# Kernel optimization log

Measured on AMD Instinct MI355X. Metric: run time of the kernel, lower is better.

Reference implementation:

```python
import jax, jax.numpy as jnp
import numpy as np

B, N, DIM, VDIM, H, HD = 4, 1369, 1024, 1536, 16, 64
ROPE_HW, ROPE_DIM, THETA = 37, 32, 10000.0
LN_EPS = 1e-5


def _rope_tables():
    # VisionRotaryEmbeddingFast: freqs_for='lang', dim=32, pt_seq_len=ft_seq_len=37
    inv = 1.0 / THETA ** (jnp.arange(0, ROPE_DIM, 2, dtype=jnp.float32) / ROPE_DIM)  # [16]
    t = jnp.arange(ROPE_HW, dtype=jnp.float32) / ROPE_HW * ROPE_HW                    # [37]
    f = t[:, None] * inv[None, :]                                                     # [37,16]
    f = jnp.repeat(f, 2, axis=-1)                                                     # [37,32]
    # broadcat along last dim over the 2D grid -> [37,37,64]
    f2 = jnp.concatenate([jnp.broadcast_to(f[:, None, :], (ROPE_HW, ROPE_HW, ROPE_DIM)),
                          jnp.broadcast_to(f[None, :, :], (ROPE_HW, ROPE_HW, ROPE_DIM))], axis=-1)
    f2 = f2.reshape(-1, 2 * ROPE_DIM)                                                 # [1369,64]
    return jnp.cos(f2), jnp.sin(f2)


def _rotate_half(x):
    # pairs (x0,x1) -> (-x1,x0), interleaved
    xr = x.reshape(*x.shape[:-1], x.shape[-1] // 2, 2)
    x1, x2 = xr[..., 0], xr[..., 1]
    return jnp.stack((-x2, x1), axis=-1).reshape(x.shape)


def setup_inputs() -> dict:
    key = jax.random.key(0)
    ks = jax.random.split(key, 8)
    return {
        "x": jax.random.normal(ks[0], (B, N, DIM), jnp.float32),
        "value": jax.random.normal(ks[1], (B, N, VDIM), jnp.float32),
        "attn_mask": jax.random.randint(ks[2], (B, N), 0, 2).astype(bool),
        "wq": jax.random.normal(ks[3], (DIM, DIM), jnp.float32) * 0.02,
        "wk": jax.random.normal(ks[4], (DIM, VDIM), jnp.float32) * 0.02,
        "wv": jax.random.normal(ks[5], (DIM, VDIM), jnp.float32) * 0.02,
        "ln_g": jnp.ones((DIM,), jnp.float32),
        "ln_b": jnp.zeros((DIM,), jnp.float32),
        "wp": jax.random.normal(ks[6], (DIM, DIM), jnp.float32) * 0.02,
        "bp": jnp.zeros((DIM,), jnp.float32),
    }


def reference(x, value, attn_mask, wq, wk, wv, ln_g, ln_b, wp, bp):
    cos, sin = _rope_tables()  # [N, 64] each
    # projections (torch F.linear: y = x @ W.T)
    q = jnp.einsum('bni,oi->bno', x, wq).reshape(B, N, H, HD).transpose(0, 2, 1, 3)
    k = jnp.einsum('bni,oi->bno', value, wk).reshape(B, N, H, HD).transpose(0, 2, 1, 3)
    v = jnp.einsum('bni,oi->bno', value, wv).reshape(B, N, H, HD).transpose(0, 2, 1, 3)
    # inline RoPE on q and k
    q = q * cos + _rotate_half(q) * sin
    k = k * cos + _rotate_half(k) * sin
    q = q * (HD ** -0.5)
    attn = jnp.einsum('bhnd,bhmd->bhnm', q, k)
    neg_inf = jnp.finfo(attn.dtype).min
    attn = jnp.where(attn_mask[:, None, None, :], attn, neg_inf)
    attn = jax.nn.softmax(attn, axis=-1)
    out = jnp.einsum('bhnm,bhmd->bhnd', attn, v)
    out = out.transpose(0, 2, 1, 3).reshape(B, N, H * HD)
    # inner_attn_ln (LayerNorm, eps=1e-5)
    mu = jnp.mean(out, axis=-1, keepdims=True)
    var = jnp.var(out, axis=-1, keepdims=True)
    out = (out - mu) * jax.lax.rsqrt(var + LN_EPS) * ln_g + ln_b
    # output projection
    return jnp.einsum('bni,oi->bno', out, wp) + bp
```

## Files before the change

kernel.cpp:

```cpp
#include <hip/hip_runtime.h>
#include <hip/hip_bf16.h>

#define BB 4
#define NN 1369
#define DIMM 1024
#define VDIMM 1536
#define HH 16
#define MM (BB*NN)
#define MPAD 5504
#define MPAD2 5632
#define NPAD 1408
#define KVB 64
#define NT (NPAD/KVB)
#define QSCALE 0.18028334f

typedef __attribute__((ext_vector_type(4))) float f32x4;
typedef __attribute__((ext_vector_type(8))) __bf16 bf16x8;
typedef __attribute__((ext_vector_type(4))) __bf16 bf16x4;

#define GLOAD_LDS(gsrc, ldst) \
  __builtin_amdgcn_global_load_lds((const __attribute__((address_space(1))) unsigned int*)(gsrc), \
                                   (__attribute__((address_space(3))) unsigned int*)(ldst), 16, 0, 0)

__global__ __launch_bounds__(256) void cvt_inputs(const float* __restrict__ x,
                                                  const float* __restrict__ val,
                                                  __bf16* __restrict__ xb,
                                                  __bf16* __restrict__ vb) {
  const int NX = MM * 1024 / 4;
  const int NV = MM * 1536 / 4;
  int i = blockIdx.x * blockDim.x + threadIdx.x;
  int st = gridDim.x * blockDim.x;
  for (; i < NX + NV; i += st) {
    const float* s; __bf16* d; int j;
    if (i < NX) { s = x; d = xb; j = i; }
    else        { s = val; d = vb; j = i - NX; }
    f32x4 v = ((const f32x4*)s)[j];
    bf16x4 o;
    o[0] = (__bf16)v[0]; o[1] = (__bf16)v[1];
    o[2] = (__bf16)v[2]; o[3] = (__bf16)v[3];
    ((bf16x4*)d)[j] = o;
  }
}

__global__ __launch_bounds__(256) void cvt_weights(
    const float* __restrict__ wq, const float* __restrict__ wk,
    const float* __restrict__ wv, const float* __restrict__ wp,
    const float* __restrict__ g,
    __bf16* __restrict__ wqb, __bf16* __restrict__ wkvb, __bf16* __restrict__ wgb) {
  const int NQ = 1024 * 1024 / 4;
  const int NK = 1024 * 1536 / 4;
  int i = blockIdx.x * blockDim.x + threadIdx.x;
  int st = gridDim.x * blockDim.x;
  for (; i < 2 * NQ + 2 * NK; i += st) {
    int j = i;
    if (j < NQ) {
      f32x4 v = ((const f32x4*)wq)[j];
      bf16x4 o;
      o[0] = (__bf16)v[0]; o[1] = (__bf16)v[1]; o[2] = (__bf16)v[2]; o[3] = (__bf16)v[3];
      ((bf16x4*)wqb)[j] = o;
    } else if (j < NQ + NK) {
      j -= NQ;
      f32x4 v = ((const f32x4*)wk)[j];
      bf16x4 o;
      o[0] = (__bf16)v[0]; o[1] = (__bf16)v[1]; o[2] = (__bf16)v[2]; o[3] = (__bf16)v[3];
      ((bf16x4*)wkvb)[j] = o;
    } else if (j < NQ + 2 * NK) {
      j -= NQ + NK;
      f32x4 v = ((const f32x4*)wv)[j];
      bf16x4 o;
      o[0] = (__bf16)v[0]; o[1] = (__bf16)v[1]; o[2] = (__bf16)v[2]; o[3] = (__bf16)v[3];
      ((bf16x4*)(wkvb + (size_t)1024 * 1536))[j] = o;
    } else {
      j -= NQ + 2 * NK;
      f32x4 v = ((const f32x4*)wp)[j];
      f32x4 gv = ((const f32x4*)g)[j & 255];
      bf16x4 o;
      o[0] = (__bf16)(v[0] * gv[0]); o[1] = (__bf16)(v[1] * gv[1]);
      o[2] = (__bf16)(v[2] * gv[2]); o[3] = (__bf16)(v[3] * gv[3]);
      ((bf16x4*)wgb)[j] = o;
    }
  }
}

__global__ __launch_bounds__(256) void c12_kernel(
    const float* __restrict__ wp, const float* __restrict__ g,
    const float* __restrict__ lnb, const float* __restrict__ bpv,
    float* __restrict__ c1, float* __restrict__ c2) {
  const int w = threadIdx.x >> 6, l = threadIdx.x & 63;
  const int o = blockIdx.x * 4 + w;
  const float* row = wp + (size_t)o * 1024;
  float s1 = 0.f, s2 = 0.f;
#pragma unroll
  for (int j = 0; j < 4; ++j) {
    const int idx = l * 4 + j * 256;
    f32x4 wv = *(const f32x4*)&row[idx];
    f32x4 gv = *(const f32x4*)&g[idx];
    f32x4 bv = *(const f32x4*)&lnb[idx];
#pragma unroll
    for (int e = 0; e < 4; ++e) { s1 += wv[e] * gv[e]; s2 += wv[e] * bv[e]; }
  }
#pragma unroll
  for (int m = 1; m < 64; m <<= 1) { s1 += __shfl_xor(s1, m); s2 += __shfl_xor(s2, m); }
  if (l == 0) { c1[o] = s1; c2[o] = s2 + bpv[o]; }
}

__global__ __launch_bounds__(256) void stats_kernel(
    const __bf16* __restrict__ AO, float* __restrict__ mu, float* __restrict__ rstd) {
  const int w = threadIdx.x >> 6, l = threadIdx.x & 63;
  const int row = blockIdx.x * 4 + w;
  const __bf16* x = AO + (size_t)row * DIMM + l * 16;
  float s = 0.f, sq = 0.f;
#pragma unroll
  for (int j = 0; j < 2; ++j) {
    bf16x8 v = *(const bf16x8*)&x[j * 8];
#pragma unroll
    for (int e = 0; e < 8; ++e) { float f = (float)v[e]; s += f; sq += f * f; }
  }
#pragma unroll
  for (int m = 1; m < 64; m <<= 1) { s += __shfl_xor(s, m); sq += __shfl_xor(sq, m); }
  if (l == 0) {
    float mean = s * (1.f / 1024.f);
    mu[row] = mean;
    rstd[row] = rsqrtf(sq * (1.f / 1024.f) - mean * mean + 1e-5f);
  }
}

__global__ __launch_bounds__(256) void prep_aux(float* __restrict__ cosT,
                                                float* __restrict__ sinT,
                                                const void* __restrict__ mask,
                                                float* __restrict__ maskA) {
  const int blk = blockIdx.x;
  if (blk < 343) {
    int idx = blk * 256 + threadIdx.x;
    if (idx >= NN * 64) return;
    int n = idx >> 6, d = idx & 63;
    int r = n / 37, c = n % 37;
    int m = (d < 32) ? (d >> 1) : ((d - 32) >> 1);
    float p = (d < 32) ? (float)r : (float)c;
    float inv = powf(10000.f, -(float)m * (1.f / 16.f));
    float a = p * inv;
    cosT[idx] = cosf(a);
    sinT[idx] = sinf(a);
  } else {
    __shared__ int flags[2];
    int t = threadIdx.x;
    if (t < 2) flags[t] = 0;
    __syncthreads();
    const unsigned int* mw = (const unsigned int*)mask;
    for (int i = t; i < NN; i += blockDim.x) {
      unsigned int w = mw[i];
      if (w == 0x3F800000u) atomicOr(&flags[1], 1);
      else if (w > 1u) atomicOr(&flags[0], 1);
    }
    __syncthreads();
    int md = flags[1] ? 2 : (flags[0] ? 1 : 0);
    const unsigned char* mb = (const unsigned char*)mask;
    const float* mf = (const float*)mask;
    for (int i = t; i < BB * NPAD; i += blockDim.x) {
      int b = i / NPAD, key = i % NPAD;
      float v = -1e30f;
      if (key < NN) {
        int idx = b * NN + key;
        bool on = (md == 0) ? (mw[idx] != 0u) : (md == 1) ? (mb[idx] != 0) : (mf[idx] != 0.f);
        if (on) v = 0.f;
      }
      maskA[i] = v;
    }
  }
}

__global__ __launch_bounds__(512, 2) void gemm_kv256(
    const __bf16* __restrict__ A, const __bf16* __restrict__ W,
    __bf16* __restrict__ Kb, __bf16* __restrict__ Vtb,
    const float* __restrict__ cosT, const float* __restrict__ sinT) {
  __shared__ __bf16 Ar[4][256 * 32];
  __shared__ __bf16 Br[4][256 * 32];
  const int tid = threadIdx.x;
  const int wid = tid >> 6, l = tid & 63;
  const int wr = wid >> 2, wc = wid & 3;
  const int lo = l & 15, hi = l >> 4;
  const int tN = blockIdx.x & 7, tM = blockIdx.x >> 3;
  const int K = VDIMM;
  const int nk = K / 32;

  const int srow = (tid >> 6) * 16 + (tid & 15);
  const int schunk = ((tid >> 4) & 3) * 8;
  const __bf16* Asrc = A + (size_t)(tM * 256 + srow) * K + schunk;
  const __bf16* Wsrc = W + (size_t)(tN * 256 + srow) * K + schunk;

  f32x4 zero = {0.f, 0.f, 0.f, 0.f};
  f32x4 acc[8][4];
#pragma unroll
  for (int i = 0; i < 8; ++i)
#pragma unroll
    for (int j = 0; j < 4; ++j) acc[i][j] = zero;

  auto GSTAGE = [&](int s, int k0) {
    GLOAD_LDS(Asrc + k0,                (char*)&Ar[s][0] + tid * 16);
    GLOAD_LDS(Asrc + (size_t)128 * K + k0, (char*)&Ar[s][0] + tid * 16 + 8192);
    GLOAD_LDS(Wsrc + k0,                (char*)&Br[s][0] + tid * 16);
    GLOAD_LDS(Wsrc + (size_t)128 * K + k0, (char*)&Br[s][0] + tid * 16 + 8192);
  };

  GSTAGE(0, 0);
  GSTAGE(1, 32);
  for (int t = 0; t < nk; ++t) {
    if (t < nk - 1) asm volatile("s_waitcnt vmcnt(4)" ::: "memory");
    else            asm volatile("s_waitcnt vmcnt(0)" ::: "memory");
    __builtin_amdgcn_s_barrier();
    const int s = t & 3;
    bf16x8 af[8], bf[4];
#pragma unroll
    for (int mi = 0; mi < 8; ++mi)
      af[mi] = *(const bf16x8*)&Ar[s][(wr * 8 + mi) * 512 + hi * 128 + lo * 8];
#pragma unroll
    for (int ni = 0; ni < 4; ++ni)
      bf[ni] = *(const bf16x8*)&Br[s][(wc * 4 + ni) * 512 + hi * 128 + lo * 8];
    if (t + 2 < nk) GSTAGE((t + 2) & 3, (t + 2) * 32);
    __builtin_amdgcn_s_setprio(1);
#pragma unroll
    for (int mi = 0; mi < 8; ++mi)
#pragma unroll
      for (int ni = 0; ni < 4; ++ni)
        acc[mi][ni] = __builtin_amdgcn_mfma_f32_16x16x32_bf16(af[mi], bf[ni], acc[mi][ni], 0, 0, 0);
    __builtin_amdgcn_s_setprio(0);
  }

  const int m_base = tM * 256 + wr * 128;
  const int o_base = tN * 256 + wc * 64;
  const bool isK = (tN < 4);
#pragma unroll
  for (int mi = 0; mi < 8; ++mi) {
    const int m4 = m_base + mi * 16 + hi * 4;
    if (!isK) {
      if (m4 < MM) {
        const int b0 = m4 / NN, n0 = m4 % NN;
#pragma unroll
        for (int ni = 0; ni < 4; ++ni) {
          const int o2 = o_base + ni * 16 + lo - 1024;
          const int h = o2 >> 6, d = o2 & 63;
          if (n0 <= NN - 4) {
            bf16x4 pv;
#pragma unroll
            for (int r = 0; r < 4; ++r) pv[r] = (__bf16)acc[mi][ni][r];
            *(bf16x4*)&Vtb[((size_t)(b0 * HH + h) * 64 + d) * NPAD + n0] = pv;
          } else {
#pragma unroll
            for (int r = 0; r < 4; ++r) {
              const int mr = m4 + r;
              const int br = mr / NN, nr = mr % NN;
              Vtb[((size_t)(br * HH + h) * 64 + d) * NPAD + nr] = (__bf16)acc[mi][ni][r];
            }
          }
        }
      }
    } else {
#pragma unroll
      for (int r = 0; r < 4; ++r) {
        const int mrow = m4 + r;
#pragma unroll
        for (int ni = 0; ni < 4; ++ni) {
          const int col = o_base + ni * 16 + lo;
          float v = acc[mi][ni][r];
          float pprt = __shfl_xor(v, 1);
          if (mrow < MM) {
            int b = mrow / NN, n = mrow % NN;
            int h = col >> 6, d = col & 63;
            float cs = cosT[n * 64 + d], sn = sinT[n * 64 + d];
            float out = v * cs + (((d & 1) == 0) ? -pprt : pprt) * sn;
            Kb[((size_t)(b * HH + h) * NPAD + n) * 64 + d] = (__bf16)out;
          }
        }
      }
    }
  }
}

template <int EPI>
__global__ __launch_bounds__(256) void gemm_bt(
    const __bf16* __restrict__ A, const __bf16* __restrict__ W, int K,
    __bf16* __restrict__ obf, float* __restrict__ of32,
    const float* __restrict__ cosT, const float* __restrict__ sinT,
    const float* __restrict__ mu, const float* __restrict__ rstd,
    const float* __restrict__ c1, const float* __restrict__ c2) {
  __shared__ __bf16 As[2][128 * 32];
  __shared__ __bf16 Bs[2][64 * 32];
  const int tid = threadIdx.x;
  const int w = tid >> 6, l = tid & 63;
  const int tN = blockIdx.x, tM = blockIdx.y;
  const int wmo = w * 32;
  const int lo = l & 15, hi = l >> 4;

  const __bf16* Asrc = A + (size_t)(tM * 128 + lo) * K + hi * 8;
  const __bf16* Wsrc = W + (size_t)(tN * 64 + lo) * K + hi * 8;

  f32x4 zero = {0.f, 0.f, 0.f, 0.f};
  f32x4 acc[2][4];
#pragma unroll
  for (int i = 0; i < 2; ++i)
#pragma unroll
    for (int j = 0; j < 4; ++j) acc[i][j] = zero;

  auto GSTAGE = [&](int buf, int k0) {
#pragma unroll
    for (int j = 0; j < 2; ++j) {
      const int c = j * 4 + w;
      GLOAD_LDS(Asrc + (size_t)c * 16 * K + k0, (char*)&As[buf][c * 512]);
    }
    GLOAD_LDS(Wsrc + (size_t)w * 16 * K + k0, (char*)&Bs[buf][w * 512]);
  };

  const int nk = K >> 5;
  GSTAGE(0, 0);
  int cur = 0;
  const int ga = wmo >> 4;
  for (int t = 0; t < nk; ++t) {
    __syncthreads();
    if (t + 1 < nk) GSTAGE(cur ^ 1, (t + 1) * 32);
    bf16x8 af[2], bfr[4];
#pragma unroll
    for (int mi = 0; mi < 2; ++mi)
      af[mi] = *(const bf16x8*)&As[cur][(ga + mi) * 512 + hi * 128 + lo * 8];
#pragma unroll
    for (int ni = 0; ni < 4; ++ni)
      bfr[ni] = *(const bf16x8*)&Bs[cur][ni * 512 + hi * 128 + lo * 8];
    __builtin_amdgcn_s_setprio(1);
#pragma unroll
    for (int mi = 0; mi < 2; ++mi)
#pragma unroll
      for (int ni = 0; ni < 4; ++ni)
        acc[mi][ni] = __builtin_amdgcn_mfma_f32_16x16x32_bf16(af[mi], bfr[ni], acc[mi][ni], 0, 0, 0);
    __builtin_amdgcn_s_setprio(0);
    cur ^= 1;
  }

  const int m_base = tM * 128 + wmo;
  const int o_base = tN * 64;
  float c1v[4], c2v[4];
  if (EPI == 3) {
#pragma unroll
    for (int ni = 0; ni < 4; ++ni) {
      c1v[ni] = c1[o_base + ni * 16 + lo];
      c2v[ni] = c2[o_base + ni * 16 + lo];
    }
  }
#pragma unroll
  for (int mi = 0; mi < 2; ++mi) {
#pragma unroll
    for (int r = 0; r < 4; ++r) {
      const int mrow = m_base + mi * 16 + hi * 4 + r;
#pragma unroll
      for (int ni = 0; ni < 4; ++ni) {
        const int col = o_base + ni * 16 + lo;
        float v = acc[mi][ni][r];
        if (EPI == 0) {
          float pprt = __shfl_xor(v, 1);
          if (mrow < MM) {
            int b = mrow / NN, n = mrow % NN;
            int h = col >> 6, d = col & 63;
            float cs = cosT[n * 64 + d], sn = sinT[n * 64 + d];
            float out = (v * cs + (((d & 1) == 0) ? -pprt : pprt) * sn) * QSCALE;
            obf[((size_t)(b * HH + h) * NPAD + n) * 64 + d] = (__bf16)out;
          }
        } else {
          if (mrow < MM)
            of32[(size_t)mrow * DIMM + col] =
                rstd[mrow] * (v - mu[mrow] * c1v[ni]) + c2v[ni];
        }
      }
    }
  }
}

__device__ inline unsigned int pk2(float a, float b) {
  unsigned int ua = (unsigned int)__builtin_bit_cast(unsigned short, (__bf16)a);
  unsigned int ub = (unsigned int)__builtin_bit_cast(unsigned short, (__bf16)b);
  return ua | (ub << 16);
}

__global__ __launch_bounds__(256) void attn_kernel(
    const __bf16* __restrict__ Qb, const __bf16* __restrict__ Kb,
    const __bf16* __restrict__ Vtb, const float* __restrict__ maskA,
    __bf16* __restrict__ AO) {
  __shared__ __bf16 Ks[2][64 * 64];
  __shared__ __bf16 Vs[2][64 * 64];
  __shared__ unsigned int Plds[4][16 * 32];
  const int tid = threadIdx.x;
  const int w = tid >> 6, l = tid & 63;
  const int lo = l & 15, hi = l >> 4;

  const int i = blockIdx.x;
  const int orig = (i & 7) * 176 + (i >> 3);
  const int bh = orig / NT;
  const int qt = orig % NT;
  const int b = bh >> 4;
  const int q0 = qt * 64 + w * 16;

  const __bf16* Qp = Qb + ((size_t)bh * NPAD + q0) * 64;
  bf16x8 qf0 = *(const bf16x8*)&Qp[lo * 64 + hi * 8];
  bf16x8 qf1 = *(const bf16x8*)&Qp[lo * 64 + 32 + hi * 8];

  const int row8 = l >> 3;
  const int swz16 = ((l & 7) ^ row8) << 4;
  const int lo7 = lo & 7;
  const int swzW = (lo & 7) << 2;

  f32x4 zero = {0.f, 0.f, 0.f, 0.f};
  f32x4 O[4];
#pragma unroll
  for (int n = 0; n < 4; ++n) O[n] = zero;
  float lr = 0.f;
  const float* mk = maskA + b * NPAD;

#define STAGE(buf, k0)                                                                   \
  {                                                                                      \
    _Pragma("unroll") for (int j = 0; j < 2; ++j) {                                      \
      const int rbase = (j * 4 + w) * 8;                                                 \
      const char* ksrc = (const char*)Kb +                                               \
          ((size_t)bh * NPAD + (k0) + rbase + row8) * 128 + swz16;                       \
      GLOAD_LDS(ksrc, (char*)&Ks[buf][0] + rbase * 128);                                 \
      const char* vsrc = (const char*)Vtb +                                              \
          ((size_t)(bh * 64 + rbase + row8) * NPAD + (k0)) * 2 + swz16;                  \
      GLOAD_LDS(vsrc, (char*)&Vs[buf][0] + rbase * 128);                                 \
    }                                                                                    \
  }

  STAGE(0, 0);
  __syncthreads();
  int cur = 0;

  for (int t = 0; t < NT; ++t) {
    if (t + 1 < NT) STAGE(cur ^ 1, (t + 1) * KVB);

    const __bf16* KB = &Ks[cur][0];
    const __bf16* VB = &Vs[cur][0];

    f32x4 mv[4];
#pragma unroll
    for (int c = 0; c < 4; ++c) mv[c] = *(const f32x4*)&mk[t * KVB + c * 16 + hi * 4];

    f32x4 S[4];
    __builtin_amdgcn_s_setprio(1);
#pragma unroll
    for (int c = 0; c < 4; ++c) {
      const int kr = c * 16 + lo;
      bf16x8 kfa = *(const bf16x8*)&KB[kr * 64 + ((hi ^ lo7) * 8)];
      bf16x8 kfb = *(const bf16x8*)&KB[kr * 64 + (((hi + 4) ^ lo7) * 8)];
      f32x4 s = __builtin_amdgcn_mfma_f32_16x16x32_bf16(kfa, qf0, zero, 0, 0, 0);
      S[c]     = __builtin_amdgcn_mfma_f32_16x16x32_bf16(kfb, qf1, s, 0, 0, 0);
    }
    __builtin_amdgcn_s_setprio(0);

    float rs = 0.f;
#pragma unroll
    for (int c = 0; c < 4; ++c) {
      float p0 = exp2f(S[c][0] + mv[c][0]);
      float p1 = exp2f(S[c][1] + mv[c][1]);
      float p2 = exp2f(S[c][2] + mv[c][2]);
      float p3 = exp2f(S[c][3] + mv[c][3]);
      rs += (p0 + p1) + (p2 + p3);
      uint2 pw = {pk2(p0, p1), pk2(p2, p3)};
      *(uint2*)&Plds[w][lo * 32 + ((8 * c + 2 * hi) ^ swzW)] = pw;
    }
    lr += rs;

    bf16x8 pf0 = *(const bf16x8*)&Plds[w][lo * 32 + ((4 * hi) ^ swzW)];
    bf16x8 pf1 = *(const bf16x8*)&Plds[w][lo * 32 + ((16 + 4 * hi) ^ swzW)];

    __builtin_amdgcn_s_setprio(1);
#pragma unroll
    for (int n = 0; n < 4; ++n) {
      const int vr = n * 16 + lo;
      bf16x8 vfa = *(const bf16x8*)&VB[vr * 64 + ((hi ^ lo7) * 8)];
      bf16x8 vfb = *(const bf16x8*)&VB[vr * 64 + (((hi + 4) ^ lo7) * 8)];
      O[n] = __builtin_amdgcn_mfma_f32_16x16x32_bf16(vfa, pf0, O[n], 0, 0, 0);
      O[n] = __builtin_amdgcn_mfma_f32_16x16x32_bf16(vfb, pf1, O[n], 0, 0, 0);
    }
    __builtin_amdgcn_s_setprio(0);

    __syncthreads();
    cur ^= 1;
  }
#undef STAGE

  lr += __shfl_xor(lr, 16);
  lr += __shfl_xor(lr, 32);
  const float inv = 1.f / lr;

  const int h = bh & 15;
  const int token = q0 + lo;
  if (token < NN) {
    __bf16* dst = AO + (size_t)(b * NN + token) * DIMM + h * 64 + hi * 4;
#pragma unroll
    for (int n = 0; n < 4; ++n) {
      bf16x4 o;
#pragma unroll
      for (int e = 0; e < 4; ++e) o[e] = (__bf16)(O[n][e] * inv);
      *(bf16x4*)(dst + n * 16) = o;
    }
  }
}

extern "C" void kernel_launch(void* const* d_in, const int* in_sizes, int n_in,
                              void* d_out, int out_size, void* d_ws, size_t ws_size,
                              hipStream_t stream) {
  const float* x   = (const float*)d_in[0];
  const float* val = (const float*)d_in[1];
  const void*  msk = d_in[2];
  const float* wq  = (const float*)d_in[3];
  const float* wk  = (const float*)d_in[4];
  const float* wv  = (const float*)d_in[5];
  const float* lng = (const float*)d_in[6];
  const float* lnb = (const float*)d_in[7];
  const float* wp  = (const float*)d_in[8];
  const float* bpv = (const float*)d_in[9];
  float* out = (float*)d_out;

  char* ws = (char*)d_ws;
  size_t off = 0;
  auto alloc = [&](size_t bytes) -> char* {
    char* p = ws + off;
    off += (bytes + 255) & ~(size_t)255;
    return p;
  };
  __bf16* xb   = (__bf16*)alloc((size_t)MPAD * 1024 * 2);
  __bf16* vb   = (__bf16*)alloc((size_t)MPAD2 * 1536 * 2);
  __bf16* wqb  = (__bf16*)alloc((size_t)1024 * 1024 * 2);
  __bf16* wkvb = (__bf16*)alloc((size_t)2048 * 1536 * 2);
  __bf16* wgb  = (__bf16*)alloc((size_t)1024 * 1024 * 2);
  __bf16* Qb   = (__bf16*)alloc((size_t)64 * NPAD * 64 * 2);
  __bf16* Kb   = (__bf16*)alloc((size_t)64 * NPAD * 64 * 2);
  __bf16* Vtb  = (__bf16*)alloc((size_t)64 * 64 * NPAD * 2);
  __bf16* AO   = (__bf16*)alloc((size_t)MPAD * 1024 * 2);
  float* cosT  = (float*)alloc((size_t)NN * 64 * 4);
  float* sinT  = (float*)alloc((size_t)NN * 64 * 4);
  float* maskA = (float*)alloc((size_t)BB * NPAD * 4);
  float* muv   = (float*)alloc((size_t)MM * 4);
  float* rstdv = (float*)alloc((size_t)MM * 4);
  float* c1v   = (float*)alloc((size_t)1024 * 4);
  float* c2v   = (float*)alloc((size_t)1024 * 4);


  cvt_inputs<<<2048, 256, 0, stream>>>(x, val, xb, vb);
  cvt_weights<<<1024, 256, 0, stream>>>(wq, wk, wv, wp, lng, wqb, wkvb, wgb);
  prep_aux<<<344, 256, 0, stream>>>(cosT, sinT, msk, maskA);
  c12_kernel<<<256, 256, 0, stream>>>(wp, lng, lnb, bpv, c1v, c2v);

  gemm_bt<0><<<dim3(16, 43), 256, 0, stream>>>(xb, wqb, 1024, Qb, nullptr,
                                               cosT, sinT, nullptr, nullptr, nullptr, nullptr);
  gemm_kv256<<<dim3(176), 512, 0, stream>>>(vb, wkvb, Kb, Vtb, cosT, sinT);

  attn_kernel<<<dim3(64 * NT), 256, 0, stream>>>(Qb, Kb, Vtb, maskA, AO);

  stats_kernel<<<MM / 4, 256, 0, stream>>>(AO, muv, rstdv);

  gemm_bt<3><<<dim3(16, 43), 256, 0, stream>>>(AO, wgb, 1024, nullptr, out,
                                               nullptr, nullptr, muv, rstdv, c1v, c2v);
}
```

Measured before the change: 263.1 us.

## Process 32 query rows per wave in attention to reuse K/V tiles

Each wave of the attention kernel now handles two 16-row query blocks instead of one, so a workgroup covers 128 queries and the grid halves. Each K and V fragment read from LDS, and each staged K/V tile, now feeds twice as many MFMAs. This cuts LDS traffic and global K/V reloads per unit of work. The cost is more registers for the doubled accumulators and S tiles, plus half as many workgroups (704), which may lower occupancy and leave CUs less evenly loaded.

```diff
diff --git a/kernel.cpp b/kernel.cpp
--- a/kernel.cpp
+++ b/kernel.cpp
@@ -12,6 +12,7 @@
 #define NPAD 1408
 #define KVB 64
 #define NT (NPAD/KVB)
+#define NT2 (NPAD/128)
 #define QSCALE 0.18028334f
 
 typedef __attribute__((ext_vector_type(4))) float f32x4;
@@ -196,9 +197,9 @@
     for (int j = 0; j < 4; ++j) acc[i][j] = zero;
 
   auto GSTAGE = [&](int s, int k0) {
-    GLOAD_LDS(Asrc + k0,                (char*)&Ar[s][0] + tid * 16);
+    GLOAD_LDS(Asrc + k0,                   (char*)&Ar[s][0] + tid * 16);
     GLOAD_LDS(Asrc + (size_t)128 * K + k0, (char*)&Ar[s][0] + tid * 16 + 8192);
-    GLOAD_LDS(Wsrc + k0,                (char*)&Br[s][0] + tid * 16);
+    GLOAD_LDS(Wsrc + k0,                   (char*)&Br[s][0] + tid * 16);
     GLOAD_LDS(Wsrc + (size_t)128 * K + k0, (char*)&Br[s][0] + tid * 16 + 8192);
   };
 
@@ -384,21 +385,23 @@
     __bf16* __restrict__ AO) {
   __shared__ __bf16 Ks[2][64 * 64];
   __shared__ __bf16 Vs[2][64 * 64];
-  __shared__ unsigned int Plds[4][16 * 32];
+  __shared__ unsigned int Plds[4][32 * 32];
   const int tid = threadIdx.x;
   const int w = tid >> 6, l = tid & 63;
   const int lo = l & 15, hi = l >> 4;
 
   const int i = blockIdx.x;
-  const int orig = (i & 7) * 176 + (i >> 3);
-  const int bh = orig / NT;
-  const int qt = orig % NT;
+  const int orig = (i & 7) * 88 + (i >> 3);
+  const int bh = orig / NT2;
+  const int qt = orig % NT2;
   const int b = bh >> 4;
-  const int q0 = qt * 64 + w * 16;
+  const int q0 = qt * 128 + w * 32;
 
   const __bf16* Qp = Qb + ((size_t)bh * NPAD + q0) * 64;
-  bf16x8 qf0 = *(const bf16x8*)&Qp[lo * 64 + hi * 8];
-  bf16x8 qf1 = *(const bf16x8*)&Qp[lo * 64 + 32 + hi * 8];
+  bf16x8 qf0a = *(const bf16x8*)&Qp[lo * 64 + hi * 8];
+  bf16x8 qf1a = *(const bf16x8*)&Qp[lo * 64 + 32 + hi * 8];
+  bf16x8 qf0b = *(const bf16x8*)&Qp[(16 + lo) * 64 + hi * 8];
+  bf16x8 qf1b = *(const bf16x8*)&Qp[(16 + lo) * 64 + 32 + hi * 8];
 
   const int row8 = l >> 3;
   const int swz16 = ((l & 7) ^ row8) << 4;
@@ -406,10 +409,10 @@
   const int swzW = (lo & 7) << 2;
 
   f32x4 zero = {0.f, 0.f, 0.f, 0.f};
-  f32x4 O[4];
-#pragma unroll
-  for (int n = 0; n < 4; ++n) O[n] = zero;
-  float lr = 0.f;
+  f32x4 O[4][2];
+#pragma unroll
+  for (int n = 0; n < 4; ++n) { O[n][0] = zero; O[n][1] = zero; }
+  float lr[2] = {0.f, 0.f};
   const float* mk = maskA + b * NPAD;
 
 #define STAGE(buf, k0)                                                                   \
@@ -439,33 +442,40 @@
 #pragma unroll
     for (int c = 0; c < 4; ++c) mv[c] = *(const f32x4*)&mk[t * KVB + c * 16 + hi * 4];
 
-    f32x4 S[4];
+    f32x4 S[4][2];
     __builtin_amdgcn_s_setprio(1);
 #pragma unroll
     for (int c = 0; c < 4; ++c) {
       const int kr = c * 16 + lo;
       bf16x8 kfa = *(const bf16x8*)&KB[kr * 64 + ((hi ^ lo7) * 8)];
       bf16x8 kfb = *(const bf16x8*)&KB[kr * 64 + (((hi + 4) ^ lo7) * 8)];
-      f32x4 s = __builtin_amdgcn_mfma_f32_16x16x32_bf16(kfa, qf0, zero, 0, 0, 0);
-      S[c]     = __builtin_amdgcn_mfma_f32_16x16x32_bf16(kfb, qf1, s, 0, 0, 0);
+      f32x4 sa = __builtin_amdgcn_mfma_f32_16x16x32_bf16(kfa, qf0a, zero, 0, 0, 0);
+      S[c][0]   = __builtin_amdgcn_mfma_f32_16x16x32_bf16(kfb, qf1a, sa, 0, 0, 0);
+      f32x4 sb = __builtin_amdgcn_mfma_f32_16x16x32_bf16(kfa, qf0b, zero, 0, 0, 0);
+      S[c][1]   = __builtin_amdgcn_mfma_f32_16x16x32_bf16(kfb, qf1b, sb, 0, 0, 0);
     }
     __builtin_amdgcn_s_setprio(0);
 
-    float rs = 0.f;
-#pragma unroll
-    for (int c = 0; c < 4; ++c) {
-      float p0 = exp2f(S[c][0] + mv[c][0]);
-      float p1 = exp2f(S[c][1] + mv[c][1]);
-      float p2 = exp2f(S[c][2] + mv[c][2]);
-      float p3 = exp2f(S[c][3] + mv[c][3]);
-      rs += (p0 + p1) + (p2 + p3);
-      uint2 pw = {pk2(p0, p1), pk2(p2, p3)};
-      *(uint2*)&Plds[w][lo * 32 + ((8 * c + 2 * hi) ^ swzW)] = pw;
-    }
-    lr += rs;
-
-    bf16x8 pf0 = *(const bf16x8*)&Plds[w][lo * 32 + ((4 * hi) ^ swzW)];
-    bf16x8 pf1 = *(const bf16x8*)&Plds[w][lo * 32 + ((16 + 4 * hi) ^ swzW)];
+#pragma unroll
+    for (int qb = 0; qb < 2; ++qb) {
+      float rs = 0.f;
+#pragma unroll
+      for (int c = 0; c < 4; ++c) {
+        float p0 = exp2f(S[c][qb][0] + mv[c][0]);
+        float p1 = exp2f(S[c][qb][1] + mv[c][1]);
+        float p2 = exp2f(S[c][qb][2] + mv[c][2]);
+        float p3 = exp2f(S[c][qb][3] + mv[c][3]);
+        rs += (p0 + p1) + (p2 + p3);
+        uint2 pw = {pk2(p0, p1), pk2(p2, p3)};
+        *(uint2*)&Plds[w][(qb * 16 + lo) * 32 + ((8 * c + 2 * hi) ^ swzW)] = pw;
+      }
+      lr[qb] += rs;
+    }
+
+    bf16x8 pf0a = *(const bf16x8*)&Plds[w][lo * 32 + ((4 * hi) ^ swzW)];
+    bf16x8 pf1a = *(const bf16x8*)&Plds[w][lo * 32 + ((16 + 4 * hi) ^ swzW)];
+    bf16x8 pf0b = *(const bf16x8*)&Plds[w][(16 + lo) * 32 + ((4 * hi) ^ swzW)];
+    bf16x8 pf1b = *(const bf16x8*)&Plds[w][(16 + lo) * 32 + ((16 + 4 * hi) ^ swzW)];
 
     __builtin_amdgcn_s_setprio(1);
 #pragma unroll
@@ -473,8 +483,10 @@
       const int vr = n * 16 + lo;
       bf16x8 vfa = *(const bf16x8*)&VB[vr * 64 + ((hi ^ lo7) * 8)];
       bf16x8 vfb = *(const bf16x8*)&VB[vr * 64 + (((hi + 4) ^ lo7) * 8)];
-      O[n] = __builtin_amdgcn_mfma_f32_16x16x32_bf16(vfa, pf0, O[n], 0, 0, 0);
-      O[n] = __builtin_amdgcn_mfma_f32_16x16x32_bf16(vfb, pf1, O[n], 0, 0, 0);
+      O[n][0] = __builtin_amdgcn_mfma_f32_16x16x32_bf16(vfa, pf0a, O[n][0], 0, 0, 0);
+      O[n][0] = __builtin_amdgcn_mfma_f32_16x16x32_bf16(vfb, pf1a, O[n][0], 0, 0, 0);
+      O[n][1] = __builtin_amdgcn_mfma_f32_16x16x32_bf16(vfa, pf0b, O[n][1], 0, 0, 0);
+      O[n][1] = __builtin_amdgcn_mfma_f32_16x16x32_bf16(vfb, pf1b, O[n][1], 0, 0, 0);
     }
     __builtin_amdgcn_s_setprio(0);
 
@@ -483,20 +495,23 @@
   }
 #undef STAGE
 
-  lr += __shfl_xor(lr, 16);
-  lr += __shfl_xor(lr, 32);
-  const float inv = 1.f / lr;
-
   const int h = bh & 15;
-  const int token = q0 + lo;
-  if (token < NN) {
-    __bf16* dst = AO + (size_t)(b * NN + token) * DIMM + h * 64 + hi * 4;
-#pragma unroll
-    for (int n = 0; n < 4; ++n) {
-      bf16x4 o;
-#pragma unroll
-      for (int e = 0; e < 4; ++e) o[e] = (__bf16)(O[n][e] * inv);
-      *(bf16x4*)(dst + n * 16) = o;
+#pragma unroll
+  for (int qb = 0; qb < 2; ++qb) {
+    float s = lr[qb];
+    s += __shfl_xor(s, 16);
+    s += __shfl_xor(s, 32);
+    const float inv = 1.f / s;
+    const int token = q0 + qb * 16 + lo;
+    if (token < NN) {
+      __bf16* dst = AO + (size_t)(b * NN + token) * DIMM + h * 64 + hi * 4;
+#pragma unroll
+      for (int n = 0; n < 4; ++n) {
+        bf16x4 o;
+#pragma unroll
+        for (int e = 0; e < 4; ++e) o[e] = (__bf16)(O[n][qb][e] * inv);
+        *(bf16x4*)(dst + n * 16) = o;
+      }
     }
   }
 }
@@ -550,7 +565,7 @@
                                                cosT, sinT, nullptr, nullptr, nullptr, nullptr);
   gemm_kv256<<<dim3(176), 512, 0, stream>>>(vb, wkvb, Kb, Vtb, cosT, sinT);
 
-  attn_kernel<<<dim3(64 * NT), 256, 0, stream>>>(Qb, Kb, Vtb, maskA, AO);
+  attn_kernel<<<dim3(64 * NT2), 256, 0, stream>>>(Qb, Kb, Vtb, maskA, AO);
 
   stats_kernel<<<MM / 4, 256, 0, stream>>>(AO, muv, rstdv);
 
```

After: 263.0 us (median of 2 runs). No clear change (-0.1%).
